# Optimization experiments

Hardware: AMD Instinct MI355X
Metric: run time of the kernel (lower is better)

The kernel has to match this reference:

```python
import jax, jax.numpy as jnp
import numpy as np

NUM_CODES = 1024
DIM = 256


def setup_inputs() -> dict:
    key = jax.random.key(0)
    k1, k2 = jax.random.split(key)
    x = jax.random.normal(k1, (16, 256, 4096), dtype=jnp.float32)
    # torch init: uniform(-1/num_codes, 1/num_codes)
    codebook = jax.random.uniform(k2, (NUM_CODES, DIM), dtype=jnp.float32,
                                  minval=-1.0 / NUM_CODES, maxval=1.0 / NUM_CODES)
    return {"x": x, "codebook": codebook}


def reference(x, codebook):
    # x: [B, C, T], codebook: [K, C]
    B, C, T = x.shape
    flat = jnp.transpose(x, (0, 2, 1)).reshape(-1, C)  # [N, C], N = B*T
    # squared L2 distances: |f|^2 - 2 f.e + |e|^2
    dist = (jnp.sum(flat * flat, axis=1, keepdims=True)
            - 2.0 * jnp.einsum('nc,kc->nk', flat, codebook)
            + jnp.sum(codebook * codebook, axis=1))  # [N, K]
    encode_idx = jnp.argmin(dist, axis=1)  # [N]
    quant = codebook[encode_idx].reshape(B, T, C).transpose(0, 2, 1)  # [B, C, T]
    # dual MSE loss (codebook + commitment, both weight 1)
    loss = (jnp.mean((jax.lax.stop_gradient(quant) - x) ** 2)
            + jnp.mean((quant - jax.lax.stop_gradient(x)) ** 2))
    # straight-through estimator
    quantized = x + jax.lax.stop_gradient(quant - x)
    return quantized, loss
```

## Files before the change

### kernel.cpp

```cpp
#include <hip/hip_runtime.h>

#define DIM 256
#define T_LEN 4096
#define K_CODES 1024
#define N_TOK 65536
#define NELEM 16777216


typedef __attribute__((ext_vector_type(8))) short bf16x8;
typedef __attribute__((ext_vector_type(16))) float f32x16;
typedef __attribute__((ext_vector_type(8))) int i32x8;

__device__ __forceinline__ unsigned short f2bf(float f) {
    unsigned u = __builtin_bit_cast(unsigned, f);
    return (unsigned short)((u + 0x7FFFu + ((u >> 16) & 1u)) >> 16);
}
__device__ __forceinline__ float bf2f(unsigned short h) {
    return __builtin_bit_cast(float, (unsigned)h << 16);
}
__device__ __forceinline__ unsigned f2u(float f) { return __builtin_bit_cast(unsigned, f); }
__device__ __forceinline__ float u2f(unsigned u) { return __builtin_bit_cast(float, u); }
__device__ __forceinline__ unsigned umin2(unsigned a, unsigned b) { return a < b ? a : b; }

union FragU { bf16x8 v; unsigned short u[8]; };

#define GLLOAD(gsrc, lbase)                                                              \
    __builtin_amdgcn_global_load_lds(                                                    \
        (const __attribute__((address_space(1))) unsigned int*)(gsrc),                   \
        (__attribute__((address_space(3))) unsigned int*)(lbase), 16, 0, 0)

__device__ __forceinline__ unsigned cvt8n(float a, float b) {
    unsigned r;
    asm("v_cvt_pk_fp8_f32 %0, -%1, -%2" : "=v"(r) : "v"(a), "v"(b));
    return r;
}
__device__ __forceinline__ unsigned cvt8(float a, float b) {
    unsigned r;
    asm("v_cvt_pk_fp8_f32 %0, %1, %2" : "=v"(r) : "v"(a), "v"(b));
    return r;
}

__global__ __launch_bounds__(256) void prep(const float* __restrict__ cb,
                                            char* __restrict__ cbb8,
                                            unsigned* __restrict__ cnh2) {
    const int k = blockIdx.x * 4 + (threadIdx.x >> 6);
    const int lane = threadIdx.x & 63;
    float4 v = *reinterpret_cast<const float4*>(cb + (size_t)k * DIM + lane * 4);
    float s = v.x * v.x + v.y * v.y + v.z * v.z + v.w * v.w;
    #pragma unroll
    for (int off = 32; off; off >>= 1) s += __shfl_down(s, off);
    if (lane == 0) {
        float cn = 128.0f + 128.0f * s;
        unsigned short chi = f2bf(cn);
        unsigned short clo = f2bf(cn - bf2f(chi));
        cnh2[k] = (unsigned)chi | ((unsigned)clo << 16);
    }
    const unsigned wlo = cvt8(256.0f * v.x, 256.0f * v.y);
    const unsigned whi = cvt8(256.0f * v.z, 256.0f * v.w);
    const unsigned dw = __builtin_amdgcn_perm(whi, wlo, 0x05040100u);
    const int d0 = lane * 4;
    const int wnd = d0 >> 6, dwi = d0 & 63, hs = dwi >> 5, i = dwi & 31;
    const int byte = (k >> 5) * 8192 + wnd * 2048 + hs * 1024 + (i >> 4) * 512
                   + (k & 31) * 16 + (i & 15);
    *reinterpret_cast<unsigned*>(cbb8 + byte) = dw;
}

__global__ __launch_bounds__(256, 2) void vq_fused(const float* __restrict__ x,
                                                   const char* __restrict__ cbb8,
                                                   const unsigned* __restrict__ cnh2,
                                                   const float* __restrict__ cbf,
                                                   float* __restrict__ out,
                                                   float* __restrict__ part) {
    __shared__ __align__(16) char ring[32768];
    __shared__ unsigned cnl[1024];
    __shared__ unsigned kbx[4][64];
    __shared__ int kkl[128];
    __shared__ float wsum[4];
    const int tid = threadIdx.x;
    const int w = tid >> 6, lane = tid & 63, hi = lane >> 5, ln31 = lane & 31;
    const int tg = w >> 1, kh = w & 1;
    const int tw0 = blockIdx.x * 128;
    const int b = tw0 >> 12, tb = tw0 & (T_LEN - 1);

    cnl[tid] = cnh2[tid];
    cnl[tid + 256] = cnh2[tid + 256];
    cnl[tid + 512] = cnh2[tid + 512];
    cnl[tid + 768] = cnh2[tid + 768];

    const int tqi = tid & 31, cqi = tid >> 5;
    const float* xb = x + (size_t)b * DIM * T_LEN + tb + 4 * tqi;
    float x2s = 0.0f;
    #pragma unroll
    for (int ii = 0; ii < 8; ++ii) {
        const int cl = (ii * 8 + cqi) * 4;
        const float* p = xb + (size_t)cl * T_LEN;
        const float4 P0 = *reinterpret_cast<const float4*>(p);
        const float4 P1 = *reinterpret_cast<const float4*>(p + T_LEN);
        const float4 P2 = *reinterpret_cast<const float4*>(p + 2 * T_LEN);
        const float4 P3 = *reinterpret_cast<const float4*>(p + 3 * T_LEN);
        x2s = fmaf(P0.x, P0.x, fmaf(P0.y, P0.y, fmaf(P0.z, P0.z, fmaf(P0.w, P0.w, x2s))));
        x2s = fmaf(P1.x, P1.x, fmaf(P1.y, P1.y, fmaf(P1.z, P1.z, fmaf(P1.w, P1.w, x2s))));
        x2s = fmaf(P2.x, P2.x, fmaf(P2.y, P2.y, fmaf(P2.z, P2.z, fmaf(P2.w, P2.w, x2s))));
        x2s = fmaf(P3.x, P3.x, fmaf(P3.y, P3.y, fmaf(P3.z, P3.z, fmaf(P3.w, P3.w, x2s))));
        const unsigned lo0 = cvt8n(P0.x, P0.y), hi0 = cvt8n(P0.z, P0.w);
        const unsigned lo1 = cvt8n(P1.x, P1.y), hi1 = cvt8n(P1.z, P1.w);
        const unsigned lo2 = cvt8n(P2.x, P2.y), hi2 = cvt8n(P2.z, P2.w);
        const unsigned lo3 = cvt8n(P3.x, P3.y), hi3 = cvt8n(P3.z, P3.w);
        const unsigned s01 = __builtin_amdgcn_perm(lo1, lo0, 0x05010400u);
        const unsigned s23 = __builtin_amdgcn_perm(lo3, lo2, 0x05010400u);
        const unsigned u01 = __builtin_amdgcn_perm(hi1, hi0, 0x05010400u);
        const unsigned u23 = __builtin_amdgcn_perm(hi3, hi2, 0x05010400u);
        const unsigned t0 = __builtin_amdgcn_perm(s23, s01, 0x05040100u);
        const unsigned t1 = __builtin_amdgcn_perm(s23, s01, 0x07060302u);
        const unsigned t2 = __builtin_amdgcn_perm(u23, u01, 0x05040100u);
        const unsigned t3 = __builtin_amdgcn_perm(u23, u01, 0x07060302u);
        const int ta = 4 * tqi;
        *reinterpret_cast<unsigned*>(ring + (ta + 0) * 256 + (cl ^ (((ta + 0) & 15) << 3))) = t0;
        *reinterpret_cast<unsigned*>(ring + (ta + 1) * 256 + (cl ^ (((ta + 1) & 15) << 3))) = t1;
        *reinterpret_cast<unsigned*>(ring + (ta + 2) * 256 + (cl ^ (((ta + 2) & 15) << 3))) = t2;
        *reinterpret_cast<unsigned*>(ring + (ta + 3) * 256 + (cl ^ (((ta + 3) & 15) << 3))) = t3;
    }
    __syncthreads();

    i32x8 xf0[4], xf1[4];
    {
        const int tp0 = tg * 64 + ln31, tp1 = tg * 64 + 32 + ln31;
        const int z0 = (tp0 & 15) << 3, z1 = (tp1 & 15) << 3;
        #pragma unroll
        for (int wnd = 0; wnd < 4; ++wnd) {
            #pragma unroll
            for (int g = 0; g < 4; ++g) {
                const int o = wnd * 64 + hi * 32 + g * 8;
                const long v0 = *reinterpret_cast<const long*>(ring + tp0 * 256 + (o ^ z0));
                const long v1 = *reinterpret_cast<const long*>(ring + tp1 * 256 + (o ^ z1));
                xf0[wnd][2 * g] = (int)(unsigned)(v0 & 0xFFFFFFFFu);
                xf0[wnd][2 * g + 1] = (int)(unsigned)(((unsigned long)v0) >> 32);
                xf1[wnd][2 * g] = (int)(unsigned)(v1 & 0xFFFFFFFFu);
                xf1[wnd][2 * g + 1] = (int)(unsigned)(((unsigned long)v1) >> 32);
            }
        }
    }
    __syncthreads();

    auto stage = [&](int kc, int buf) {
        char* lb = ring + buf * 16384 + w * 1024;
        const char* gc = cbb8 + kc * 8192;
        #pragma unroll
        for (int j = 0; j < 4; ++j) {
            const int o = j * 4096 + tid * 16;
            GLLOAD(gc + (o & 8191) + (o >> 13) * 131072, lb + j * 4096);
        }
    };
    stage(0, 0);

    FragU cfr0, onef;
    #pragma unroll
    for (int i = 0; i < 8; ++i) onef.u[i] = (hi == 0 && i < 2) ? 0x3F80 : 0;

    unsigned b0a = 0xFFFFFFFFu, b0b = 0xFFFFFFFFu;
    unsigned b1a = 0xFFFFFFFFu, b1b = 0xFFFFFFFFu;

    for (int kc = 0; kc < 16; ++kc) {
        const int cur = kc & 1;
        if (kc < 15) {
            stage(kc + 1, cur ^ 1);
            asm volatile("s_waitcnt vmcnt(4)" ::: "memory");
        } else {
            asm volatile("s_waitcnt vmcnt(0)" ::: "memory");
        }
        __builtin_amdgcn_s_barrier();
        __builtin_amdgcn_sched_barrier(0);

        const unsigned d = cnl[kh * 512 + kc * 32 + ln31];
        #pragma unroll
        for (int i = 0; i < 8; ++i) cfr0.u[i] = 0;
        if (hi == 0) {
            cfr0.u[0] = (unsigned short)(d & 0xFFFFu);
            cfr0.u[1] = (unsigned short)(d >> 16);
        }

        f32x16 acc0, acc1;
        #pragma unroll
        for (int i = 0; i < 16; ++i) { acc0[i] = 0.0f; acc1[i] = 0.0f; }
        acc0 = __builtin_amdgcn_mfma_f32_32x32x16_bf16(cfr0.v, onef.v, acc0, 0, 0, 0);
        acc1 = __builtin_amdgcn_mfma_f32_32x32x16_bf16(cfr0.v, onef.v, acc1, 0, 0, 0);

        const char* cbpA = ring + cur * 16384 + kh * 8192 + hi * 1024 + ln31 * 16;
        #pragma unroll
        for (int wnd = 0; wnd < 4; ++wnd) {
            const uint4 alo = *reinterpret_cast<const uint4*>(cbpA + wnd * 2048);
            const uint4 ahi = *reinterpret_cast<const uint4*>(cbpA + wnd * 2048 + 512);
            i32x8 aw;
            aw[0] = (int)alo.x; aw[1] = (int)alo.y; aw[2] = (int)alo.z; aw[3] = (int)alo.w;
            aw[4] = (int)ahi.x; aw[5] = (int)ahi.y; aw[6] = (int)ahi.z; aw[7] = (int)ahi.w;
            acc0 = __builtin_amdgcn_mfma_scale_f32_32x32x64_f8f6f4(
                aw, xf0[wnd], acc0, 0, 0, 0, 0x7F7F7F7F, 0, 0x7F7F7F7F);
            acc1 = __builtin_amdgcn_mfma_scale_f32_32x32x64_f8f6f4(
                aw, xf1[wnd], acc1, 0, 0, 0, 0x7F7F7F7F, 0, 0x7F7F7F7F);
        }

        const int kbl = kh * 512 + kc * 32 + hi * 4;
        #pragma unroll
        for (int rg = 0; rg < 16; ++rg) {
            const unsigned kk = (unsigned)(kbl + (rg & 3) + 8 * (rg >> 2));
            const unsigned p0 = (f2u(acc0[rg]) & 0xFFFFFC00u) | kk;
            const unsigned p1 = (f2u(acc1[rg]) & 0xFFFFFC00u) | kk;
            if (rg & 1) { b0b = umin2(b0b, p0); b1b = umin2(b1b, p1); }
            else        { b0a = umin2(b0a, p0); b1a = umin2(b1a, p1); }
        }
        __builtin_amdgcn_s_barrier();
        __builtin_amdgcn_sched_barrier(0);
    }

    unsigned best0 = umin2(b0a, b0b);
    unsigned best1 = umin2(b1a, b1b);
    best0 = umin2(best0, __shfl_xor(best0, 32));
    best1 = umin2(best1, __shfl_xor(best1, 32));
    if (hi == 0) { kbx[w][ln31] = best0; kbx[w][32 + ln31] = best1; }
    __syncthreads();

    float red = x2s;
    if (kh == 0) {
        const unsigned key = umin2(kbx[w][lane], kbx[w + 1][lane]);
        kkl[tg * 64 + lane] = (int)(key & 1023u);
        red += (u2f(key & 0xFFFFFC00u) - 128.0f) * 0.0078125f;
    }
    #pragma unroll
    for (int off = 32; off; off >>= 1) red += __shfl_down(red, off);
    if (lane == 0) wsum[w] = red;
    __syncthreads();
    if (tid == 0) part[blockIdx.x] = wsum[0] + wsum[1] + wsum[2] + wsum[3];

    float* fs = (float*)ring;
    const int tt = tid & 127, ch = tid >> 7;
    const size_t rowb = (size_t)kkl[tt] * DIM;
    #pragma unroll 1
    for (int sl = 0; sl < 8; ++sl) {
        float4 g[4];
        #pragma unroll
        for (int i = 0; i < 4; ++i)
            g[i] = *reinterpret_cast<const float4*>(cbf + rowb + sl * 32 + ch * 16 + 4 * i);
        __syncthreads();
        #pragma unroll
        for (int i = 0; i < 4; ++i) {
            const int c0 = ch * 16 + 4 * i;
            fs[(c0 + 0) * 132 + tt] = g[i].x;
            fs[(c0 + 1) * 132 + tt] = g[i].y;
            fs[(c0 + 2) * 132 + tt] = g[i].z;
            fs[(c0 + 3) * 132 + tt] = g[i].w;
        }
        __syncthreads();
        #pragma unroll
        for (int p = 0; p < 4; ++p) {
            const int c = tid >> 3, tq = (tid & 7) + p * 8;
            const float4 v = *reinterpret_cast<const float4*>(fs + c * 132 + tq * 4);
            *reinterpret_cast<float4*>(
                out + (((size_t)(b * DIM + sl * 32 + c)) << 12) + tb + tq * 4) = v;
        }
    }
}

__global__ __launch_bounds__(256) void finalize(const float* __restrict__ part,
                                                float* __restrict__ loss_out) {
    double s = (double)part[threadIdx.x] + (double)part[threadIdx.x + 256];
    #pragma unroll
    for (int off = 32; off; off >>= 1) s += __shfl_down(s, off);
    __shared__ double wsum[4];
    const int lane = threadIdx.x & 63, wv = threadIdx.x >> 6;
    if (lane == 0) wsum[wv] = s;
    __syncthreads();
    if (threadIdx.x == 0)
        *loss_out = (float)(2.0 * (wsum[0] + wsum[1] + wsum[2] + wsum[3]) / (double)NELEM);
}

extern "C" void kernel_launch(void* const* d_in, const int* in_sizes, int n_in,
                              void* d_out, int out_size, void* d_ws, size_t ws_size,
                              hipStream_t stream) {
    const float* x  = (const float*)d_in[0];
    const float* cb = (const float*)d_in[1];
    float* out = (float*)d_out;
    unsigned* ws = (unsigned*)d_ws;
    unsigned* cnh2 = ws;
    float* part = (float*)(ws + 1024);
    char* cbb8 = (char*)(ws + 4096);

    prep<<<K_CODES / 4, 256, 0, stream>>>(cb, cbb8, cnh2);
    vq_fused<<<N_TOK / 128, 256, 0, stream>>>(x, cbb8, cnh2, cb, out, part);
    finalize<<<1, 256, 0, stream>>>(part, out + NELEM);
}
```

Baseline: 49.30 us.

## Triple-buffer codebook ring, split MFMA chains, fold loss into atomics

The codebook staging ring grows from two to three buffers, so the barrier at the end of each iteration can be dropped and the next chunk can be prefetched without a WAR hazard. The four fp8 MFMAs per token tile are split across two independent accumulator chains (P/Q) whose results are summed afterwards, which shortens the dependent MFMA chain. The separate finalize kernel is replaced by a memset plus a per-block float atomicAdd, removing one launch. In exchange LDS use per block rises by 16 KB, which may affect occupancy, and the loss reduction becomes float atomics in nondeterministic order rather than a double-precision sum.

Result: slower. 56.86 us (+15.3%).

```diff
diff --git a/kernel.cpp b/kernel.cpp
--- a/kernel.cpp
+++ b/kernel.cpp
@@ -70,8 +70,8 @@
                                                    const unsigned* __restrict__ cnh2,
                                                    const float* __restrict__ cbf,
                                                    float* __restrict__ out,
-                                                   float* __restrict__ part) {
-    __shared__ __align__(16) char ring[32768];
+                                                   float* __restrict__ loss) {
+    __shared__ __align__(16) char ring[49152];
     __shared__ unsigned cnl[1024];
     __shared__ unsigned kbx[4][64];
     __shared__ int kkl[128];
@@ -153,7 +153,7 @@
     };
     stage(0, 0);
 
-    FragU cfr0, onef;
+    FragU onef;
     #pragma unroll
     for (int i = 0; i < 8; ++i) onef.u[i] = (hi == 0 && i < 2) ? 0x3F80 : 0;
 
@@ -161,9 +161,9 @@
     unsigned b1a = 0xFFFFFFFFu, b1b = 0xFFFFFFFFu;
 
     for (int kc = 0; kc < 16; ++kc) {
-        const int cur = kc & 1;
+        const int cur = kc % 3;
         if (kc < 15) {
-            stage(kc + 1, cur ^ 1);
+            stage(kc + 1, (kc + 1) % 3);
             asm volatile("s_waitcnt vmcnt(4)" ::: "memory");
         } else {
             asm volatile("s_waitcnt vmcnt(0)" ::: "memory");
@@ -172,6 +172,7 @@
         __builtin_amdgcn_sched_barrier(0);
 
         const unsigned d = cnl[kh * 512 + kc * 32 + ln31];
+        FragU cfr0;
         #pragma unroll
         for (int i = 0; i < 8; ++i) cfr0.u[i] = 0;
         if (hi == 0) {
@@ -179,37 +180,50 @@
             cfr0.u[1] = (unsigned short)(d >> 16);
         }
 
-        f32x16 acc0, acc1;
-        #pragma unroll
-        for (int i = 0; i < 16; ++i) { acc0[i] = 0.0f; acc1[i] = 0.0f; }
-        acc0 = __builtin_amdgcn_mfma_f32_32x32x16_bf16(cfr0.v, onef.v, acc0, 0, 0, 0);
-        acc1 = __builtin_amdgcn_mfma_f32_32x32x16_bf16(cfr0.v, onef.v, acc1, 0, 0, 0);
-
         const char* cbpA = ring + cur * 16384 + kh * 8192 + hi * 1024 + ln31 * 16;
+        i32x8 aw[4];
         #pragma unroll
         for (int wnd = 0; wnd < 4; ++wnd) {
             const uint4 alo = *reinterpret_cast<const uint4*>(cbpA + wnd * 2048);
             const uint4 ahi = *reinterpret_cast<const uint4*>(cbpA + wnd * 2048 + 512);
-            i32x8 aw;
-            aw[0] = (int)alo.x; aw[1] = (int)alo.y; aw[2] = (int)alo.z; aw[3] = (int)alo.w;
-            aw[4] = (int)ahi.x; aw[5] = (int)ahi.y; aw[6] = (int)ahi.z; aw[7] = (int)ahi.w;
-            acc0 = __builtin_amdgcn_mfma_scale_f32_32x32x64_f8f6f4(
-                aw, xf0[wnd], acc0, 0, 0, 0, 0x7F7F7F7F, 0, 0x7F7F7F7F);
-            acc1 = __builtin_amdgcn_mfma_scale_f32_32x32x64_f8f6f4(
-                aw, xf1[wnd], acc1, 0, 0, 0, 0x7F7F7F7F, 0, 0x7F7F7F7F);
-        }
+            aw[wnd][0] = (int)alo.x; aw[wnd][1] = (int)alo.y;
+            aw[wnd][2] = (int)alo.z; aw[wnd][3] = (int)alo.w;
+            aw[wnd][4] = (int)ahi.x; aw[wnd][5] = (int)ahi.y;
+            aw[wnd][6] = (int)ahi.z; aw[wnd][7] = (int)ahi.w;
+        }
+
+        f32x16 accP0, accQ0, accP1, accQ1;
+        #pragma unroll
+        for (int i = 0; i < 16; ++i) { accP0[i] = 0.0f; accQ0[i] = 0.0f;
+                                       accP1[i] = 0.0f; accQ1[i] = 0.0f; }
+        accP0 = __builtin_amdgcn_mfma_f32_32x32x16_bf16(cfr0.v, onef.v, accP0, 0, 0, 0);
+        accP1 = __builtin_amdgcn_mfma_f32_32x32x16_bf16(cfr0.v, onef.v, accP1, 0, 0, 0);
+        accQ0 = __builtin_amdgcn_mfma_scale_f32_32x32x64_f8f6f4(
+            aw[2], xf0[2], accQ0, 0, 0, 0, 0x7F7F7F7F, 0, 0x7F7F7F7F);
+        accQ1 = __builtin_amdgcn_mfma_scale_f32_32x32x64_f8f6f4(
+            aw[2], xf1[2], accQ1, 0, 0, 0, 0x7F7F7F7F, 0, 0x7F7F7F7F);
+        accP0 = __builtin_amdgcn_mfma_scale_f32_32x32x64_f8f6f4(
+            aw[0], xf0[0], accP0, 0, 0, 0, 0x7F7F7F7F, 0, 0x7F7F7F7F);
+        accP1 = __builtin_amdgcn_mfma_scale_f32_32x32x64_f8f6f4(
+            aw[0], xf1[0], accP1, 0, 0, 0, 0x7F7F7F7F, 0, 0x7F7F7F7F);
+        accQ0 = __builtin_amdgcn_mfma_scale_f32_32x32x64_f8f6f4(
+            aw[3], xf0[3], accQ0, 0, 0, 0, 0x7F7F7F7F, 0, 0x7F7F7F7F);
+        accQ1 = __builtin_amdgcn_mfma_scale_f32_32x32x64_f8f6f4(
+            aw[3], xf1[3], accQ1, 0, 0, 0, 0x7F7F7F7F, 0, 0x7F7F7F7F);
+        accP0 = __builtin_amdgcn_mfma_scale_f32_32x32x64_f8f6f4(
+            aw[1], xf0[1], accP0, 0, 0, 0, 0x7F7F7F7F, 0, 0x7F7F7F7F);
+        accP1 = __builtin_amdgcn_mfma_scale_f32_32x32x64_f8f6f4(
+            aw[1], xf1[1], accP1, 0, 0, 0, 0x7F7F7F7F, 0, 0x7F7F7F7F);
 
         const int kbl = kh * 512 + kc * 32 + hi * 4;
         #pragma unroll
         for (int rg = 0; rg < 16; ++rg) {
             const unsigned kk = (unsigned)(kbl + (rg & 3) + 8 * (rg >> 2));
-            const unsigned p0 = (f2u(acc0[rg]) & 0xFFFFFC00u) | kk;
-            const unsigned p1 = (f2u(acc1[rg]) & 0xFFFFFC00u) | kk;
+            const unsigned p0 = (f2u(accP0[rg] + accQ0[rg]) & 0xFFFFFC00u) | kk;
+            const unsigned p1 = (f2u(accP1[rg] + accQ1[rg]) & 0xFFFFFC00u) | kk;
             if (rg & 1) { b0b = umin2(b0b, p0); b1b = umin2(b1b, p1); }
             else        { b0a = umin2(b0a, p0); b1a = umin2(b1a, p1); }
         }
-        __builtin_amdgcn_s_barrier();
-        __builtin_amdgcn_sched_barrier(0);
     }
 
     unsigned best0 = umin2(b0a, b0b);
@@ -229,7 +243,8 @@
     for (int off = 32; off; off >>= 1) red += __shfl_down(red, off);
     if (lane == 0) wsum[w] = red;
     __syncthreads();
-    if (tid == 0) part[blockIdx.x] = wsum[0] + wsum[1] + wsum[2] + wsum[3];
+    if (tid == 0)
+        atomicAdd(loss, (wsum[0] + wsum[1] + wsum[2] + wsum[3]) * (2.0f / (float)NELEM));
 
     float* fs = (float*)ring;
     const int tt = tid & 127, ch = tid >> 7;
@@ -258,19 +273,6 @@
                 out + (((size_t)(b * DIM + sl * 32 + c)) << 12) + tb + tq * 4) = v;
         }
     }
-}
-
-__global__ __launch_bounds__(256) void finalize(const float* __restrict__ part,
-                                                float* __restrict__ loss_out) {
-    double s = (double)part[threadIdx.x] + (double)part[threadIdx.x + 256];
-    #pragma unroll
-    for (int off = 32; off; off >>= 1) s += __shfl_down(s, off);
-    __shared__ double wsum[4];
-    const int lane = threadIdx.x & 63, wv = threadIdx.x >> 6;
-    if (lane == 0) wsum[wv] = s;
-    __syncthreads();
-    if (threadIdx.x == 0)
-        *loss_out = (float)(2.0 * (wsum[0] + wsum[1] + wsum[2] + wsum[3]) / (double)NELEM);
 }
 
 extern "C" void kernel_launch(void* const* d_in, const int* in_sizes, int n_in,
@@ -281,10 +283,9 @@
     float* out = (float*)d_out;
     unsigned* ws = (unsigned*)d_ws;
     unsigned* cnh2 = ws;
-    float* part = (float*)(ws + 1024);
     char* cbb8 = (char*)(ws + 4096);
 
+    hipMemsetAsync(out + NELEM, 0, 4, stream);
     prep<<<K_CODES / 4, 256, 0, stream>>>(cb, cbb8, cnh2);
-    vq_fused<<<N_TOK / 128, 256, 0, stream>>>(x, cbb8, cnh2, cb, out, part);
-    finalize<<<1, 256, 0, stream>>>(part, out + NELEM);
-}
+    vq_fused<<<N_TOK / 128, 256, 0, stream>>>(x, cbb8, cnh2, cb, out, out + NELEM);
+}
```
